# Performance work log

Hardware: AMD Instinct MI355X
Metric: run time of the kernel (lower is better)

## Reference

```python
import jax, jax.numpy as jnp
import numpy as np
import math

NUM_HEADS = 16
EPS = 1e-5

# Single-step spikingjelly LIFNode(tau=2.0, v_threshold=1.0, v_reset=0.0):
#   v = (x - 0)/tau = x/2 ; spike = heaviside(v - 1) = (x >= 2)
@jax.custom_vjp
def lif(x):
    return (x >= 2.0).astype(x.dtype)

def _lif_fwd(x):
    return (x >= 2.0).astype(x.dtype), x

def _lif_bwd(x, g):
    # sigmoid surrogate (alpha=4) on v - v_th, chained through dv/dx = 1/tau = 0.5
    s = jax.nn.sigmoid(4.0 * (0.5 * x - 1.0))
    return (g * (4.0 * s * (1.0 - s)) * 0.5,)

lif.defvjp(_lif_fwd, _lif_bwd)

def layernorm(x, gamma, beta):
    mu = jnp.mean(x, axis=-1, keepdims=True)
    var = jnp.var(x, axis=-1, keepdims=True)
    return (x - mu) * jax.lax.rsqrt(var + EPS) * gamma + beta

def mish(x):
    return x * jnp.tanh(jax.nn.softplus(x))

def setup_inputs() -> dict:
    key = jax.random.key(0)
    ks = jax.random.split(key, 8)
    B, Sq, Skv, dQ, dK, dV = 8, 1024, 1024, 1024, 1024, 1024
    def xavier_normal(k, shape):
        std = math.sqrt(2.0 / (shape[0] + shape[1]))
        return jax.random.normal(k, shape, jnp.float32) * std
    return {
        "Q": jax.random.normal(ks[0], (B, Sq, dQ), jnp.float32) * 2.0,
        "K": jax.random.normal(ks[1], (B, Skv, dK), jnp.float32) * 2.0,
        "adj_mask": (jax.random.uniform(ks[2], (B, 1, Sq, Skv)) < 0.7).astype(jnp.float32),
        "Wq": xavier_normal(ks[3], (dV, dQ)), "bq": jnp.zeros((dV,), jnp.float32),
        "Wk": xavier_normal(ks[4], (dV, dK)), "bk": jnp.zeros((dV,), jnp.float32),
        "Wv": xavier_normal(ks[5], (dV, dK)), "bv": jnp.zeros((dV,), jnp.float32),
        "Wo": xavier_normal(ks[6], (dV, dV)), "bo": jnp.zeros((dV,), jnp.float32),
        "g_q": jnp.ones((dV,), jnp.float32), "be_q": jnp.zeros((dV,), jnp.float32),
        "g_k": jnp.ones((dV,), jnp.float32), "be_k": jnp.zeros((dV,), jnp.float32),
    }

def reference(Q, K, adj_mask, Wq, bq, Wk, bk, Wv, bv, Wo, bo, g_q, be_q, g_k, be_k):
    B, Sq, _ = Q.shape
    Skv = K.shape[1]
    dV = Wq.shape[0]
    hd = dV // NUM_HEADS
    # LIF-gated projections (eval mode: dropout off)
    q = lif(layernorm(lif(Q) @ Wq.T + bq, g_q, be_q))          # [B,Sq,dV] binary
    v = lif(K) @ Wv.T + bv                                      # fc_v(k_lif(K))
    k = lif(layernorm(lif(K) @ Wk.T + bk, g_k, be_k))          # K(k_norm(fc_k(v_lif(K))))
    q = q.reshape(B, Sq, NUM_HEADS, hd).transpose(0, 2, 1, 3)  # [B,H,Sq,hd]
    k = k.reshape(B, Skv, NUM_HEADS, hd).transpose(0, 2, 1, 3)
    v = v.reshape(B, Skv, NUM_HEADS, hd).transpose(0, 2, 1, 3)
    scores = jnp.einsum('bhqd,bhkd->bhqk', q, k) / math.sqrt(hd)
    scores = scores * adj_mask                                  # multiplicative mask
    w = jax.nn.softmax(scores, axis=-1)
    out = jnp.einsum('bhqk,bhkd->bhqd', w, v)
    out = out.transpose(0, 2, 1, 3).reshape(B, Sq, dV)
    o = out @ Wo.T + bo
    return out + mish(o)
```

## Files before the change

kernel.cpp:

```cpp
#include <hip/hip_runtime.h>
#include <hip/hip_bf16.h>

typedef __attribute__((ext_vector_type(4))) float fx4;
typedef __attribute__((ext_vector_type(8))) short bv8;
typedef unsigned int u32;
typedef unsigned short u16;
typedef __hip_bfloat16 bf16;

#define DEVI static __device__ __forceinline__

static constexpr int NBATCH = 8;
static constexpr int SEQ = 1024;
static constexpr int DM  = 1024;
static constexpr int NH  = 16;
static constexpr int MROWS = NBATCH * SEQ;
static constexpr size_t SZ = (size_t)MROWS * DM;

DEVI void gl16(const void* g, void* l) {
  __builtin_amdgcn_global_load_lds((const __attribute__((address_space(1))) void*)g,
                                   (__attribute__((address_space(3))) void*)l, 16, 0, 0);
}
DEVI fx4 mfma_bf16(bv8 a, bv8 b, fx4 c) {
  return __builtin_amdgcn_mfma_f32_16x16x32_bf16(a, b, c, 0, 0, 0);
}

__global__ __launch_bounds__(256) void prep_weights(
    const float* __restrict__ wq, const float* __restrict__ wk,
    const float* __restrict__ wv, const float* __restrict__ wo,
    bf16* __restrict__ qe, bf16* __restrict__ ke,
    bf16* __restrict__ vb, bf16* __restrict__ ob)
{
  int i = (blockIdx.x * 256 + threadIdx.x) * 4;
  int w = blockIdx.y;
  const float* src = (w == 0) ? wq : (w == 1) ? wk : (w == 2) ? wv : wo;
  fx4 v = *(const fx4*)&src[i];
  if (w < 2) {
    bf16* dst = (w == 0) ? qe : ke;
    int col = i >> 10, k = i & 1023;
    size_t base = (size_t)col * 3072 + k;
    bf16 hi[4], mi[4], lo[4];
#pragma unroll
    for (int j = 0; j < 4; j++) {
      float x = v[j];
      bf16 h = __float2bfloat16(x);
      float r1 = x - __bfloat162float(h);
      bf16 m = __float2bfloat16(r1);
      float r2 = r1 - __bfloat162float(m);
      hi[j] = h; mi[j] = m; lo[j] = __float2bfloat16(r2);
    }
    *(uint2*)&dst[base]        = *(const uint2*)hi;
    *(uint2*)&dst[base + 1024] = *(const uint2*)mi;
    *(uint2*)&dst[base + 2048] = *(const uint2*)lo;
  } else {
    bf16* dst = (w == 2) ? vb : ob;
    bf16 t[4];
#pragma unroll
    for (int j = 0; j < 4; j++) t[j] = __float2bfloat16(v[j]);
    *(uint2*)&dst[i] = *(const uint2*)t;
  }
}

__global__ __launch_bounds__(256) void spike_kernel(const float* __restrict__ x, u16* __restrict__ o)
{
  size_t i = ((size_t)blockIdx.x * 256 + threadIdx.x) * 4;
  fx4 v = *(const fx4*)&x[i];
  u32 a = (v[0] >= 2.f ? 0x3F80u : 0u) | ((v[1] >= 2.f ? 0x3F80u : 0u) << 16);
  u32 b = (v[2] >= 2.f ? 0x3F80u : 0u) | ((v[3] >= 2.f ? 0x3F80u : 0u) << 16);
  u32* p = (u32*)(o + i);
  p[0] = a; p[1] = b;
}

__global__ __launch_bounds__(256) void maskpack_kernel(const float* __restrict__ m, u32* __restrict__ w)
{
  size_t gid = (size_t)blockIdx.x * 256 + threadIdx.x;
  unsigned long long bal = __ballot(m[gid] != 0.0f);
  int lane = threadIdx.x & 63;
  u32 skv = (u32)(gid & 1023);
  u32 sq  = (u32)((gid >> 10) & 1023);
  u32 b   = (u32)(gid >> 20);
  size_t oidx = (size_t)b * 32768 + (skv >> 5) * 1024 + sq;
  if (lane == 0) w[oidx] = (u32)bal;
  else if (lane == 32) w[oidx] = (u32)(bal >> 32);
}

template<int EPI>
__global__ __launch_bounds__(256) void gemm_bt(
    const bf16* __restrict__ A, const bf16* __restrict__ B,
    const float* __restrict__ bias, const float* __restrict__ addsrc,
    float* __restrict__ Cf, bf16* __restrict__ Cb, int K, int N)
{
  __shared__ __attribute__((aligned(16))) bf16 sA[128 * 64];
  __shared__ __attribute__((aligned(16))) bf16 sB[128 * 64];
  const int tid = threadIdx.x;
  const int lane = tid & 63, wave = tid >> 6;
  const int wr = wave >> 1, wc = wave & 1;
  const int l15 = lane & 15, l4 = lane >> 4;
  const int rowBase = blockIdx.x * 128;
  const int colBase = blockIdx.y * 128;

  fx4 acc[4][4];
#pragma unroll
  for (int m = 0; m < 4; m++) {
#pragma unroll
    for (int n = 0; n < 4; n++) acc[m][n] = fx4{0.f, 0.f, 0.f, 0.f};
  }

  for (int kt = 0; kt < K; kt += 64) {
    const int ka = kt & 1023;
#pragma unroll
    for (int i = 0; i < 4; i++) {
      int c = i * 256 + tid;
      int r = c >> 3, cb = (c & 7) * 8;
      gl16(A + (size_t)(rowBase + r) * 1024 + ka + cb, &sA[c * 8]);
    }
#pragma unroll
    for (int i = 0; i < 4; i++) {
      int c = i * 256 + tid;
      int r = c >> 3, cb = (c & 7) * 8;
      gl16(B + (size_t)(colBase + r) * K + kt + cb, &sB[c * 8]);
    }
    __syncthreads();
#pragma unroll
    for (int kk = 0; kk < 2; kk++) {
      bv8 af[4];
#pragma unroll
      for (int m = 0; m < 4; m++)
        af[m] = *(const bv8*)&sA[(wr * 64 + m * 16 + l15) * 64 + kk * 32 + l4 * 8];
#pragma unroll
      for (int n = 0; n < 4; n++) {
        bv8 bfr = *(const bv8*)&sB[(wc * 64 + n * 16 + l15) * 64 + kk * 32 + l4 * 8];
#pragma unroll
        for (int m = 0; m < 4; m++) acc[m][n] = mfma_bf16(af[m], bfr, acc[m][n]);
      }
    }
    __syncthreads();
  }
#pragma unroll
  for (int n = 0; n < 4; n++) {
    int col = colBase + wc * 64 + n * 16 + l15;
    float bvv = bias[col];
#pragma unroll
    for (int m = 0; m < 4; m++) {
      int row0 = rowBase + wr * 64 + m * 16 + l4 * 4;
      if (EPI == 3) {
        bf16 t[4];
#pragma unroll
        for (int r = 0; r < 4; r++) t[r] = __float2bfloat16(acc[m][n][r] + bvv);
        size_t idx = (size_t)(row0 >> 10) * SEQ * DM + (size_t)col * SEQ + (row0 & 1023);
        *(uint2*)&Cb[idx] = *(const uint2*)t;
      } else {
#pragma unroll
        for (int r = 0; r < 4; r++) {
          size_t idx = (size_t)(row0 + r) * N + col;
          float val = acc[m][n][r] + bvv;
          if (EPI == 0) {
            Cf[idx] = val;
          } else {
            float u = __expf(val);
            float num = u * (u + 2.0f);
            float mish = val * num / (num + 2.0f);
            Cf[idx] = addsrc[idx] + mish;
          }
        }
      }
    }
  }
}

__global__ __launch_bounds__(256) void lnlif_kernel(
    const float* __restrict__ x, const float* __restrict__ g, const float* __restrict__ be,
    u16* __restrict__ out)
{
  __shared__ float red[4];
  const int row = blockIdx.x;
  const int tid = threadIdx.x;
  fx4 v = *(const fx4*)&x[(size_t)row * DM + tid * 4];
  float s = v[0] + v[1] + v[2] + v[3];
#pragma unroll
  for (int off = 1; off < 64; off <<= 1) s += __shfl_xor(s, off, 64);
  if ((tid & 63) == 0) red[tid >> 6] = s;
  __syncthreads();
  float mean = (red[0] + red[1] + red[2] + red[3]) * (1.0f / 1024.0f);
  __syncthreads();
  float d0 = v[0] - mean, d1 = v[1] - mean, d2 = v[2] - mean, d3 = v[3] - mean;
  float ss = d0 * d0 + d1 * d1 + d2 * d2 + d3 * d3;
#pragma unroll
  for (int off = 1; off < 64; off <<= 1) ss += __shfl_xor(ss, off, 64);
  if ((tid & 63) == 0) red[tid >> 6] = ss;
  __syncthreads();
  float var = (red[0] + red[1] + red[2] + red[3]) * (1.0f / 1024.0f);
  float rstd = rsqrtf(var + 1e-5f);
  const int c = tid * 4;
  fx4 gg = *(const fx4*)&g[c];
  fx4 bb = *(const fx4*)&be[c];
  float y0 = d0 * rstd * gg[0] + bb[0];
  float y1 = d1 * rstd * gg[1] + bb[1];
  float y2 = d2 * rstd * gg[2] + bb[2];
  float y3 = d3 * rstd * gg[3] + bb[3];
  u32 a = (y0 >= 2.f ? 0x3F80u : 0u) | ((y1 >= 2.f ? 0x3F80u : 0u) << 16);
  u32 b = (y2 >= 2.f ? 0x3F80u : 0u) | ((y3 >= 2.f ? 0x3F80u : 0u) << 16);
  u32* p = (u32*)(out + (size_t)row * DM + c);
  p[0] = a; p[1] = b;
}

__global__ __launch_bounds__(256) void attn_kernel(
    const bf16* __restrict__ qb, const bf16* __restrict__ kb, const bf16* __restrict__ vt,
    const u32* __restrict__ mwT, float* __restrict__ of, bf16* __restrict__ ob)
{
  __shared__ __attribute__((aligned(16))) bf16 sK[2][64 * 64];
  __shared__ __attribute__((aligned(16))) bf16 sV[2][64 * 64];
  __shared__ __attribute__((aligned(16))) bf16 sP[4][16 * 64];
  __shared__ __attribute__((aligned(16))) u32 sM[2][128];
  const int qt = blockIdx.x, h = blockIdx.y, b = blockIdx.z;
  const int tid = threadIdx.x, lane = tid & 63, wave = tid >> 6;
  const int l15 = lane & 15, l4 = lane >> 4;
  const size_t qrow0 = (size_t)b * SEQ + qt * 64;
  const bf16* kB = kb + (size_t)b * SEQ * DM + h * 64;
  const bf16* vB = vt + (size_t)b * SEQ * DM + (size_t)(h * 64) * SEQ;
  const u32*  mB = mwT + (size_t)b * 32768 + qt * 64;

  auto STAGE = [&](int t, int buf) {
    const int kvb = t * 64;
#pragma unroll
    for (int i = 0; i < 2; i++) {
      int c = i * 256 + tid;
      int row = c >> 3;
      int sb = ((c & 7) * 16) ^ ((row & 7) << 4);
      gl16(kB + (size_t)(kvb + row) * DM + (sb >> 1), &sK[buf][c * 8]);
      gl16(vB + (size_t)row * SEQ + kvb + (sb >> 1), &sV[buf][c * 8]);
    }
    if (tid < 32) {
      int w = tid >> 4, rg = (tid & 15) * 4;
      uint4 mv = *(const uint4*)&mB[(size_t)(t * 2 + w) * 1024 + rg];
      *(uint4*)&sM[buf][w * 64 + rg] = mv;
    }
  };

  bv8 af[2];
#pragma unroll
  for (int kk = 0; kk < 2; kk++)
    af[kk] = *(const bv8*)&qb[(qrow0 + wave * 16 + l15) * DM + h * 64 + kk * 32 + l4 * 8];

  fx4 acc_o[4];
#pragma unroll
  for (int n = 0; n < 4; n++) acc_o[n] = fx4{0.f, 0.f, 0.f, 0.f};
  float psum[4] = {0.f, 0.f, 0.f, 0.f};

  char* sPw = (char*)sP[wave];
  STAGE(0, 0);

  for (int t = 0; t < 16; t++) {
    const int cur = t & 1;
    asm volatile("s_waitcnt vmcnt(0) lgkmcnt(0)" ::: "memory");
    __builtin_amdgcn_s_barrier();
    if (t < 15) STAGE(t + 1, cur ^ 1);

    const char* sKc = (const char*)sK[cur];
    const char* sVc = (const char*)sV[cur];

    fx4 accs[4];
#pragma unroll
    for (int n = 0; n < 4; n++) accs[n] = fx4{0.f, 0.f, 0.f, 0.f};
    __builtin_amdgcn_s_setprio(1);
#pragma unroll
    for (int kk = 0; kk < 2; kk++) {
#pragma unroll
      for (int n = 0; n < 4; n++) {
        int row = n * 16 + l15;
        bv8 bk8 = *(const bv8*)(sKc + row * 128 + ((kk * 64 + l4 * 16) ^ ((row & 7) << 4)));
        accs[n] = mfma_bf16(af[kk], bk8, accs[n]);
      }
    }
    __builtin_amdgcn_s_setprio(0);

    uint4 m0 = *(const uint4*)&sM[cur][wave * 16 + l4 * 4];
    uint4 m1 = *(const uint4*)&sM[cur][64 + wave * 16 + l4 * 4];
    u32 sh0[4] = {m0.x >> l15, m0.y >> l15, m0.z >> l15, m0.w >> l15};
    u32 sh1[4] = {m1.x >> l15, m1.y >> l15, m1.z >> l15, m1.w >> l15};

#pragma unroll
    for (int n = 0; n < 4; n++) {
#pragma unroll
      for (int r = 0; r < 4; r++) {
        float e = exp2f(accs[n][r] * 0.18033688011112042f);
        u32 s = (n < 2) ? sh0[r] : sh1[r];
        float p = ((s >> ((n & 1) * 16)) & 1u) ? e : 1.0f;
        psum[r] += p;
        int pr = l4 * 4 + r;
        int cb = (n * 16 + l15) * 2;
        *(bf16*)(sPw + pr * 128 + (cb ^ ((pr & 7) << 4))) = __float2bfloat16(p);
      }
    }

    __builtin_amdgcn_s_setprio(1);
#pragma unroll
    for (int kk = 0; kk < 2; kk++) {
      bv8 pa = *(const bv8*)(sPw + l15 * 128 + ((kk * 64 + l4 * 16) ^ ((l15 & 7) << 4)));
#pragma unroll
      for (int n = 0; n < 4; n++) {
        int row = n * 16 + l15;
        bv8 bv8v = *(const bv8*)(sVc + row * 128 + ((kk * 64 + l4 * 16) ^ ((row & 7) << 4)));
        acc_o[n] = mfma_bf16(pa, bv8v, acc_o[n]);
      }
    }
    __builtin_amdgcn_s_setprio(0);
  }

#pragma unroll
  for (int r = 0; r < 4; r++) {
    float t2 = psum[r];
    t2 += __shfl_xor(t2, 1, 64);
    t2 += __shfl_xor(t2, 2, 64);
    t2 += __shfl_xor(t2, 4, 64);
    t2 += __shfl_xor(t2, 8, 64);
    float inv = 1.0f / t2;
    size_t row = qrow0 + wave * 16 + (l4 << 2) + r;
#pragma unroll
    for (int n = 0; n < 4; n++) {
      size_t idx = row * DM + h * 64 + n * 16 + l15;
      float val = acc_o[n][r] * inv;
      of[idx] = val;
      ob[idx] = __float2bfloat16(val);
    }
  }
}

extern "C" void kernel_launch(void* const* d_in, const int* in_sizes, int n_in,
                              void* d_out, int out_size, void* d_ws, size_t ws_size,
                              hipStream_t stream) {
  (void)in_sizes; (void)n_in; (void)out_size; (void)ws_size;
  const float* Q    = (const float*)d_in[0];
  const float* Kin  = (const float*)d_in[1];
  const float* mask = (const float*)d_in[2];
  const float* Wq   = (const float*)d_in[3];
  const float* bq   = (const float*)d_in[4];
  const float* Wk   = (const float*)d_in[5];
  const float* bk   = (const float*)d_in[6];
  const float* Wv   = (const float*)d_in[7];
  const float* bv   = (const float*)d_in[8];
  const float* Wo   = (const float*)d_in[9];
  const float* bo   = (const float*)d_in[10];
  const float* g_q  = (const float*)d_in[11];
  const float* be_q = (const float*)d_in[12];
  const float* g_k  = (const float*)d_in[13];
  const float* be_k = (const float*)d_in[14];
  float* out = (float*)d_out;

  char* w = (char*)d_ws;
  size_t off = 0;
  auto alloc = [&](size_t bytes) -> char* {
    char* p = w + off;
    off += (bytes + 255) & ~(size_t)255;
    return p;
  };
  bf16* q_spike = (bf16*)alloc(SZ * 2);
  bf16* k_spike = (bf16*)alloc(SZ * 2);
  float* xq     = (float*)alloc(SZ * 4);
  float* xk     = (float*)alloc(SZ * 4);
  bf16* vtb     = (bf16*)alloc(SZ * 2);
  u32* mwords   = (u32*)alloc(SZ / 32 * 4);
  bf16* wqe = (bf16*)alloc((size_t)DM * DM * 3 * 2);
  bf16* wke = (bf16*)alloc((size_t)DM * DM * 3 * 2);
  bf16* wvb = (bf16*)alloc((size_t)DM * DM * 2);
  bf16* wob = (bf16*)alloc((size_t)DM * DM * 2);
  bf16* qbn = q_spike;
  bf16* kbn = k_spike;
  float* attn_out = xq;
  bf16* attn_outb = (bf16*)xk;

  prep_weights<<<dim3(DM * DM / 1024, 4), 256, 0, stream>>>(Wq, Wk, Wv, Wo, wqe, wke, wvb, wob);
  spike_kernel<<<SZ / 1024, 256, 0, stream>>>(Q, (u16*)q_spike);
  spike_kernel<<<SZ / 1024, 256, 0, stream>>>(Kin, (u16*)k_spike);
  maskpack_kernel<<<SZ / 256, 256, 0, stream>>>(mask, mwords);

  gemm_bt<0><<<dim3(64, 8), 256, 0, stream>>>(q_spike, wqe, bq, nullptr, xq, nullptr, 3072, DM);
  gemm_bt<0><<<dim3(64, 8), 256, 0, stream>>>(k_spike, wke, bk, nullptr, xk, nullptr, 3072, DM);
  gemm_bt<3><<<dim3(64, 8), 256, 0, stream>>>(k_spike, wvb, bv, nullptr, nullptr, vtb, 1024, DM);

  lnlif_kernel<<<MROWS, 256, 0, stream>>>(xq, g_q, be_q, (u16*)qbn);
  lnlif_kernel<<<MROWS, 256, 0, stream>>>(xk, g_k, be_k, (u16*)kbn);

  attn_kernel<<<dim3(16, NH, NBATCH), 256, 0, stream>>>(qbn, kbn, vtb, mwords, attn_out, attn_outb);

  gemm_bt<2><<<dim3(64, 8), 256, 0, stream>>>(attn_outb, wob, bo, attn_out, out, nullptr, 1024, DM);
}
```

Before: 505.3 us.

## Merge paired launches and transpose score MFMA for packed softmax stores

Combines the Q/K spike, Q/K projection GEMM and Q/K layernorm launches into single grid launches indexed by blockIdx, which cuts launch count and tail effects. Splits the templated GEMM into specialized kernels. The V GEMM now uses swapped MFMA operands to change the epilogue write pattern. In attention, the score MFMA operands are swapped so each lane holds four consecutive keys for one query row. This lets probabilities be packed with v_cvt_pk_bf16 into 8-byte LDS stores and the row sum to be reduced with fewer shuffles. The V transposed epilogue now does scalar 2-byte strided stores instead of 8-byte vector stores, which may cost more.

```diff
diff --git a/kernel.cpp b/kernel.cpp
--- a/kernel.cpp
+++ b/kernel.cpp
@@ -22,6 +22,11 @@
 }
 DEVI fx4 mfma_bf16(bv8 a, bv8 b, fx4 c) {
   return __builtin_amdgcn_mfma_f32_16x16x32_bf16(a, b, c, 0, 0, 0);
+}
+DEVI u32 cvt_pk_bf16(float a, float b) {
+  u32 r;
+  asm("v_cvt_pk_bf16_f32 %0, %1, %2" : "=v"(r) : "v"(a), "v"(b));
+  return r;
 }
 
 __global__ __launch_bounds__(256) void prep_weights(
@@ -60,8 +65,12 @@
   }
 }
 
-__global__ __launch_bounds__(256) void spike_kernel(const float* __restrict__ x, u16* __restrict__ o)
-{
+__global__ __launch_bounds__(256) void spike2_kernel(
+    const float* __restrict__ xq, const float* __restrict__ xk,
+    u16* __restrict__ oq, u16* __restrict__ ok)
+{
+  const float* x = blockIdx.y ? xk : xq;
+  u16* o = blockIdx.y ? ok : oq;
   size_t i = ((size_t)blockIdx.x * 256 + threadIdx.x) * 4;
   fx4 v = *(const fx4*)&x[i];
   u32 a = (v[0] >= 2.f ? 0x3F80u : 0u) | ((v[1] >= 2.f ? 0x3F80u : 0u) << 16);
@@ -83,11 +92,79 @@
   else if (lane == 32) w[oidx] = (u32)(bal >> 32);
 }
 
-template<int EPI>
-__global__ __launch_bounds__(256) void gemm_bt(
+__global__ __launch_bounds__(256) void gemm_qk(
+    const bf16* __restrict__ Aq, const bf16* __restrict__ Ak,
+    const bf16* __restrict__ Bq, const bf16* __restrict__ Bk,
+    const float* __restrict__ biq, const float* __restrict__ bik,
+    float* __restrict__ Cq, float* __restrict__ Ck)
+{
+  __shared__ __attribute__((aligned(16))) bf16 sA[128 * 64];
+  __shared__ __attribute__((aligned(16))) bf16 sB[128 * 64];
+  const int z = blockIdx.z;
+  const bf16* A = z ? Ak : Aq;
+  const bf16* B = z ? Bk : Bq;
+  const float* bias = z ? bik : biq;
+  float* Cf = z ? Ck : Cq;
+  const int tid = threadIdx.x;
+  const int lane = tid & 63, wave = tid >> 6;
+  const int wr = wave >> 1, wc = wave & 1;
+  const int l15 = lane & 15, l4 = lane >> 4;
+  const int rowBase = blockIdx.x * 128;
+  const int colBase = blockIdx.y * 128;
+
+  fx4 acc[4][4];
+#pragma unroll
+  for (int m = 0; m < 4; m++)
+#pragma unroll
+    for (int n = 0; n < 4; n++) acc[m][n] = fx4{0.f, 0.f, 0.f, 0.f};
+
+  for (int kt = 0; kt < 3072; kt += 64) {
+    const int ka = kt & 1023;
+#pragma unroll
+    for (int i = 0; i < 4; i++) {
+      int c = i * 256 + tid;
+      int r = c >> 3, cb = (c & 7) * 8;
+      gl16(A + (size_t)(rowBase + r) * 1024 + ka + cb, &sA[c * 8]);
+    }
+#pragma unroll
+    for (int i = 0; i < 4; i++) {
+      int c = i * 256 + tid;
+      int r = c >> 3, cb = (c & 7) * 8;
+      gl16(B + (size_t)(colBase + r) * 3072 + kt + cb, &sB[c * 8]);
+    }
+    __syncthreads();
+#pragma unroll
+    for (int kk = 0; kk < 2; kk++) {
+      bv8 af[4];
+#pragma unroll
+      for (int m = 0; m < 4; m++)
+        af[m] = *(const bv8*)&sA[(wr * 64 + m * 16 + l15) * 64 + kk * 32 + l4 * 8];
+#pragma unroll
+      for (int n = 0; n < 4; n++) {
+        bv8 bfr = *(const bv8*)&sB[(wc * 64 + n * 16 + l15) * 64 + kk * 32 + l4 * 8];
+#pragma unroll
+        for (int m = 0; m < 4; m++) acc[m][n] = mfma_bf16(af[m], bfr, acc[m][n]);
+      }
+    }
+    __syncthreads();
+  }
+#pragma unroll
+  for (int n = 0; n < 4; n++) {
+    int col = colBase + wc * 64 + n * 16 + l15;
+    float bvv = bias[col];
+#pragma unroll
+    for (int m = 0; m < 4; m++) {
+      int row0 = rowBase + wr * 64 + m * 16 + l4 * 4;
+#pragma unroll
+      for (int r = 0; r < 4; r++)
+        Cf[(size_t)(row0 + r) * DM + col] = acc[m][n][r] + bvv;
+    }
+  }
+}
+
+__global__ __launch_bounds__(256) void gemm_vT(
     const bf16* __restrict__ A, const bf16* __restrict__ B,
-    const float* __restrict__ bias, const float* __restrict__ addsrc,
-    float* __restrict__ Cf, bf16* __restrict__ Cb, int K, int N)
+    const float* __restrict__ bias, bf16* __restrict__ VT)
 {
   __shared__ __attribute__((aligned(16))) bf16 sA[128 * 64];
   __shared__ __attribute__((aligned(16))) bf16 sB[128 * 64];
@@ -100,24 +177,88 @@
 
   fx4 acc[4][4];
 #pragma unroll
-  for (int m = 0; m < 4; m++) {
+  for (int m = 0; m < 4; m++)
 #pragma unroll
     for (int n = 0; n < 4; n++) acc[m][n] = fx4{0.f, 0.f, 0.f, 0.f};
-  }
-
-  for (int kt = 0; kt < K; kt += 64) {
-    const int ka = kt & 1023;
+
+  for (int kt = 0; kt < 1024; kt += 64) {
 #pragma unroll
     for (int i = 0; i < 4; i++) {
       int c = i * 256 + tid;
       int r = c >> 3, cb = (c & 7) * 8;
-      gl16(A + (size_t)(rowBase + r) * 1024 + ka + cb, &sA[c * 8]);
+      gl16(A + (size_t)(rowBase + r) * 1024 + kt + cb, &sA[c * 8]);
     }
 #pragma unroll
     for (int i = 0; i < 4; i++) {
       int c = i * 256 + tid;
       int r = c >> 3, cb = (c & 7) * 8;
-      gl16(B + (size_t)(colBase + r) * K + kt + cb, &sB[c * 8]);
+      gl16(B + (size_t)(colBase + r) * 1024 + kt + cb, &sB[c * 8]);
+    }
+    __syncthreads();
+#pragma unroll
+    for (int kk = 0; kk < 2; kk++) {
+      bv8 af[4];
+#pragma unroll
+      for (int m = 0; m < 4; m++)
+        af[m] = *(const bv8*)&sA[(wr * 64 + m * 16 + l15) * 64 + kk * 32 + l4 * 8];
+#pragma unroll
+      for (int n = 0; n < 4; n++) {
+        bv8 bfr = *(const bv8*)&sB[(wc * 64 + n * 16 + l15) * 64 + kk * 32 + l4 * 8];
+#pragma unroll
+        for (int m = 0; m < 4; m++) acc[m][n] = mfma_bf16(bfr, af[m], acc[m][n]);
+      }
+    }
+    __syncthreads();
+  }
+  const int b = rowBase >> 10;
+  const int tokb = rowBase & 1023;
+#pragma unroll
+  for (int n = 0; n < 4; n++) {
+#pragma unroll
+    for (int m = 0; m < 4; m++) {
+      int token = tokb + wr * 64 + m * 16 + l15;
+#pragma unroll
+      for (int e = 0; e < 4; e++) {
+        int wcol = colBase + wc * 64 + n * 16 + l4 * 4 + e;
+        float val = acc[m][n][e] + bias[wcol];
+        VT[(size_t)b * SEQ * DM + (size_t)wcol * SEQ + token] = __float2bfloat16(val);
+      }
+    }
+  }
+}
+
+__global__ __launch_bounds__(256) void gemm_o(
+    const bf16* __restrict__ A, const bf16* __restrict__ B,
+    const float* __restrict__ bias, const float* __restrict__ addsrc,
+    float* __restrict__ Cf)
+{
+  __shared__ __attribute__((aligned(16))) bf16 sA[128 * 64];
+  __shared__ __attribute__((aligned(16))) bf16 sB[128 * 64];
+  const int tid = threadIdx.x;
+  const int lane = tid & 63, wave = tid >> 6;
+  const int wr = wave >> 1, wc = wave & 1;
+  const int l15 = lane & 15, l4 = lane >> 4;
+  const int rowBase = blockIdx.x * 128;
+  const int colBase = blockIdx.y * 128;
+
+  fx4 acc[4][4];
+#pragma unroll
+  for (int m = 0; m < 4; m++)
+#pragma unroll
+    for (int n = 0; n < 4; n++) acc[m][n] = fx4{0.f, 0.f, 0.f, 0.f};
+
+  for (int kt = 0; kt < 1024; kt += 64) {
+#pragma unroll
+    for (int i = 0; i < 4; i++) {
+      int c = i * 256 + tid;
+      int r = c >> 3, cb = (c & 7) * 8;
+      gl16(A + (size_t)(rowBase + r) * 1024 + kt + cb, &sA[c * 8]);
+    }
+#pragma unroll
+    for (int i = 0; i < 4; i++) {
+      int c = i * 256 + tid;
+      int r = c >> 3, cb = (c & 7) * 8;
+      gl16(B + (size_t)(colBase + r) * 1024 + kt + cb, &sB[c * 8]);
     }
     __syncthreads();
 #pragma unroll
@@ -142,35 +283,29 @@
 #pragma unroll
     for (int m = 0; m < 4; m++) {
       int row0 = rowBase + wr * 64 + m * 16 + l4 * 4;
-      if (EPI == 3) {
-        bf16 t[4];
-#pragma unroll
-        for (int r = 0; r < 4; r++) t[r] = __float2bfloat16(acc[m][n][r] + bvv);
-        size_t idx = (size_t)(row0 >> 10) * SEQ * DM + (size_t)col * SEQ + (row0 & 1023);
-        *(uint2*)&Cb[idx] = *(const uint2*)t;
-      } else {
-#pragma unroll
-        for (int r = 0; r < 4; r++) {
-          size_t idx = (size_t)(row0 + r) * N + col;
-          float val = acc[m][n][r] + bvv;
-          if (EPI == 0) {
-            Cf[idx] = val;
-          } else {
-            float u = __expf(val);
-            float num = u * (u + 2.0f);
-            float mish = val * num / (num + 2.0f);
-            Cf[idx] = addsrc[idx] + mish;
-          }
-        }
-      }
-    }
-  }
-}
-
-__global__ __launch_bounds__(256) void lnlif_kernel(
-    const float* __restrict__ x, const float* __restrict__ g, const float* __restrict__ be,
-    u16* __restrict__ out)
-{
+#pragma unroll
+      for (int r = 0; r < 4; r++) {
+        size_t idx = (size_t)(row0 + r) * DM + col;
+        float val = acc[m][n][r] + bvv;
+        float u = __expf(val);
+        float num = u * (u + 2.0f);
+        Cf[idx] = addsrc[idx] + val * num / (num + 2.0f);
+      }
+    }
+  }
+}
+
+__global__ __launch_bounds__(256) void lnlif2_kernel(
+    const float* __restrict__ xq, const float* __restrict__ xk,
+    const float* __restrict__ gq, const float* __restrict__ beq,
+    const float* __restrict__ gk, const float* __restrict__ bek,
+    u16* __restrict__ outq, u16* __restrict__ outk)
+{
+  const int z = blockIdx.y;
+  const float* x = z ? xk : xq;
+  const float* g = z ? gk : gq;
+  const float* be = z ? bek : beq;
+  u16* out = z ? outk : outq;
   __shared__ float red[4];
   const int row = blockIdx.x;
   const int tid = threadIdx.x;
@@ -236,17 +371,18 @@
     }
   };
 
-  bv8 af[2];
+  bv8 qf[2];
 #pragma unroll
   for (int kk = 0; kk < 2; kk++)
-    af[kk] = *(const bv8*)&qb[(qrow0 + wave * 16 + l15) * DM + h * 64 + kk * 32 + l4 * 8];
+    qf[kk] = *(const bv8*)&qb[(qrow0 + wave * 16 + l15) * DM + h * 64 + kk * 32 + l4 * 8];
 
   fx4 acc_o[4];
 #pragma unroll
   for (int n = 0; n < 4; n++) acc_o[n] = fx4{0.f, 0.f, 0.f, 0.f};
-  float psum[4] = {0.f, 0.f, 0.f, 0.f};
+  float psum = 0.f;
 
   char* sPw = (char*)sP[wave];
+  const int swzq = (l15 & 7) << 4;
   STAGE(0, 0);
 
   for (int t = 0; t < 16; t++) {
@@ -267,53 +403,55 @@
 #pragma unroll
       for (int n = 0; n < 4; n++) {
         int row = n * 16 + l15;
-        bv8 bk8 = *(const bv8*)(sKc + row * 128 + ((kk * 64 + l4 * 16) ^ ((row & 7) << 4)));
-        accs[n] = mfma_bf16(af[kk], bk8, accs[n]);
+        bv8 kf = *(const bv8*)(sKc + row * 128 + ((kk * 64 + l4 * 16) ^ ((row & 7) << 4)));
+        accs[n] = mfma_bf16(kf, qf[kk], accs[n]);
       }
     }
     __builtin_amdgcn_s_setprio(0);
 
-    uint4 m0 = *(const uint4*)&sM[cur][wave * 16 + l4 * 4];
-    uint4 m1 = *(const uint4*)&sM[cur][64 + wave * 16 + l4 * 4];
-    u32 sh0[4] = {m0.x >> l15, m0.y >> l15, m0.z >> l15, m0.w >> l15};
-    u32 sh1[4] = {m1.x >> l15, m1.y >> l15, m1.z >> l15, m1.w >> l15};
+    u32 m0 = sM[cur][wave * 16 + l15];
+    u32 m1 = sM[cur][64 + wave * 16 + l15];
+    u32 tb[4] = {m0 >> (l4 * 4), m0 >> (16 + l4 * 4), m1 >> (l4 * 4), m1 >> (16 + l4 * 4)};
 
 #pragma unroll
     for (int n = 0; n < 4; n++) {
-#pragma unroll
-      for (int r = 0; r < 4; r++) {
-        float e = exp2f(accs[n][r] * 0.18033688011112042f);
-        u32 s = (n < 2) ? sh0[r] : sh1[r];
-        float p = ((s >> ((n & 1) * 16)) & 1u) ? e : 1.0f;
-        psum[r] += p;
-        int pr = l4 * 4 + r;
-        int cb = (n * 16 + l15) * 2;
-        *(bf16*)(sPw + pr * 128 + (cb ^ ((pr & 7) << 4))) = __float2bfloat16(p);
-      }
+      float p0, p1, p2, p3;
+      {
+        float e0 = exp2f(accs[n][0] * 0.18033688011112042f);
+        float e1 = exp2f(accs[n][1] * 0.18033688011112042f);
+        float e2 = exp2f(accs[n][2] * 0.18033688011112042f);
+        float e3 = exp2f(accs[n][3] * 0.18033688011112042f);
+        p0 = (tb[n] & 1u) ? e0 : 1.0f;
+        p1 = ((tb[n] >> 1) & 1u) ? e1 : 1.0f;
+        p2 = ((tb[n] >> 2) & 1u) ? e2 : 1.0f;
+        p3 = ((tb[n] >> 3) & 1u) ? e3 : 1.0f;
+      }
+      psum += (p0 + p1) + (p2 + p3);
+      uint2 pk;
+      pk.x = cvt_pk_bf16(p0, p1);
+      pk.y = cvt_pk_bf16(p2, p3);
+      *(uint2*)(sPw + l15 * 128 + ((n * 32 + l4 * 8) ^ swzq)) = pk;
     }
 
     __builtin_amdgcn_s_setprio(1);
 #pragma unroll
     for (int kk = 0; kk < 2; kk++) {
-      bv8 pa = *(const bv8*)(sPw + l15 * 128 + ((kk * 64 + l4 * 16) ^ ((l15 & 7) << 4)));
+      bv8 pa = *(const bv8*)(sPw + l15 * 128 + ((kk * 64 + l4 * 16) ^ swzq));
 #pragma unroll
       for (int n = 0; n < 4; n++) {
         int row = n * 16 + l15;
-        bv8 bv8v = *(const bv8*)(sVc + row * 128 + ((kk * 64 + l4 * 16) ^ ((row & 7) << 4)));
-        acc_o[n] = mfma_bf16(pa, bv8v, acc_o[n]);
+        bv8 vf = *(const bv8*)(sVc + row * 128 + ((kk * 64 + l4 * 16) ^ ((row & 7) << 4)));
+        acc_o[n] = mfma_bf16(pa, vf, acc_o[n]);
       }
     }
     __builtin_amdgcn_s_setprio(0);
   }
 
+  psum += __shfl_xor(psum, 16, 64);
+  psum += __shfl_xor(psum, 32, 64);
 #pragma unroll
   for (int r = 0; r < 4; r++) {
-    float t2 = psum[r];
-    t2 += __shfl_xor(t2, 1, 64);
-    t2 += __shfl_xor(t2, 2, 64);
-    t2 += __shfl_xor(t2, 4, 64);
-    t2 += __shfl_xor(t2, 8, 64);
-    float inv = 1.0f / t2;
+    float inv = 1.0f / __shfl(psum, l4 * 4 + r, 64);
     size_t row = qrow0 + wave * 16 + (l4 << 2) + r;
 #pragma unroll
     for (int n = 0; n < 4; n++) {
@@ -369,18 +507,16 @@
   bf16* attn_outb = (bf16*)xk;
 
   prep_weights<<<dim3(DM * DM / 1024, 4), 256, 0, stream>>>(Wq, Wk, Wv, Wo, wqe, wke, wvb, wob);
-  spike_kernel<<<SZ / 1024, 256, 0, stream>>>(Q, (u16*)q_spike);
-  spike_kernel<<<SZ / 1024, 256, 0, stream>>>(Kin, (u16*)k_spike);
+  spike2_kernel<<<dim3(SZ / 1024, 2), 256, 0, stream>>>(Q, Kin, (u16*)q_spike, (u16*)k_spike);
   maskpack_kernel<<<SZ / 256, 256, 0, stream>>>(mask, mwords);
 
-  gemm_bt<0><<<dim3(64, 8), 256, 0, stream>>>(q_spike, wqe, bq, nullptr, xq, nullptr, 3072, DM);
-  gemm_bt<0><<<dim3(64, 8), 256, 0, stream>>>(k_spike, wke, bk, nullptr, xk, nullptr, 3072, DM);
-  gemm_bt<3><<<dim3(64, 8), 256, 0, stream>>>(k_spike, wvb, bv, nullptr, nullptr, vtb, 1024, DM);
-
-  lnlif_kernel<<<MROWS, 256, 0, stream>>>(xq, g_q, be_q, (u16*)qbn);
-  lnlif_kernel<<<MROWS, 256, 0, stream>>>(xk, g_k, be_k, (u16*)kbn);
+  gemm_qk<<<dim3(64, 8, 2), 256, 0, stream>>>(q_spike, k_spike, wqe, wke, bq, bk, xq, xk);
+  gemm_vT<<<dim3(64, 8), 256, 0, stream>>>(k_spike, wvb, bv, vtb);
+
+  lnlif2_kernel<<<dim3(MROWS, 2), 256, 0, stream>>>(xq, xk, g_q, be_q, g_k, be_k,
+                                                    (u16*)qbn, (u16*)kbn);
 
   attn_kernel<<<dim3(16, NH, NBATCH), 256, 0, stream>>>(qbn, kbn, vtb, mwords, attn_out, attn_outb);
 
-  gemm_bt<2><<<dim3(64, 8), 256, 0, stream>>>(attn_outb, wob, bo, attn_out, out, nullptr, 1024, DM);
-}
+  gemm_o<<<dim3(64, 8), 256, 0, stream>>>(attn_outb, wob, bo, attn_out, out);
+}
```

New measurement: 476.3 us. 5.7% less time.
